# Performance work log

Measured on AMD Instinct MI355X. Metric: run time of the kernel, lower is better.

## Reference

```python
import jax, jax.numpy as jnp
import numpy as np

N, E, G = 50000, 400000, 256   # nodes, edges, graphs
DIN, DH = 513, 128             # int(256*4/2+1), dim_h
BN_EPS = 1e-5

def _lin_init(k, fin, fout):
    k1, k2 = jax.random.split(k)
    s = 1.0 / np.sqrt(fin)
    w = jax.random.uniform(k1, (fin, fout), jnp.float32, -s, s)
    b = jax.random.uniform(k2, (fout,), jnp.float32, -s, s)
    return w, b

def setup_inputs():
    ks = list(jax.random.split(jax.random.key(0), 20))
    inp = {
        'x': jax.random.normal(ks[0], (N, DIN), jnp.float32),
        'edge_index': jax.random.randint(ks[1], (2, E), 0, N),
        'batch': jnp.sort(jax.random.randint(ks[2], (N,), 0, G)),
    }
    i = 3
    for c in (1, 2, 3):
        fin = DIN if c == 1 else DH
        w1, b1 = _lin_init(ks[i], fin, DH); i += 1
        w2, b2 = _lin_init(ks[i], DH, DH); i += 1
        inp['conv%d_w1' % c], inp['conv%d_b1' % c] = w1, b1
        inp['conv%d_bn_g' % c] = jnp.ones((DH,), jnp.float32)
        inp['conv%d_bn_b' % c] = jnp.zeros((DH,), jnp.float32)
        inp['conv%d_bn_m' % c] = 0.1 * jax.random.normal(ks[i], (DH,), jnp.float32); i += 1
        inp['conv%d_bn_v' % c] = jax.random.uniform(ks[i], (DH,), jnp.float32, 0.5, 1.5); i += 1
        inp['conv%d_w2' % c], inp['conv%d_b2' % c] = w2, b2
    inp['lin1_w'], inp['lin1_b'] = _lin_init(ks[i], 3 * DH, 3 * DH); i += 1
    inp['lin2_w'], inp['lin2_b'] = _lin_init(ks[i], 3 * DH, 3)
    return inp

def _gin_conv(x, src, dst, w1, b1, g, bb, m, v, w2, b2):
    # GINConv, eps=0: MLP((1+eps)*x + sum_{j->i} x_j)
    agg = jax.ops.segment_sum(x[src], dst, num_segments=x.shape[0])
    h = (x + agg) @ w1 + b1
    h = (h - m) * jax.lax.rsqrt(v + BN_EPS) * g + bb   # BatchNorm1d (eval, running stats)
    h = jax.nn.relu(h)
    return jax.nn.relu(h @ w2 + b2)

def _mean_pool(h, batch, num_graphs):
    s = jax.ops.segment_sum(h, batch, num_segments=num_graphs)
    cnt = jax.ops.segment_sum(jnp.ones((h.shape[0],), h.dtype), batch, num_segments=num_graphs)
    return s / jnp.maximum(cnt, 1.0)[:, None]

def reference(x, edge_index, batch, conv1_w1, conv1_b1, conv1_bn_g, conv1_bn_b, conv1_bn_m, conv1_bn_v, conv1_w2, conv1_b2, conv2_w1, conv2_b1, conv2_bn_g, conv2_bn_b, conv2_bn_m, conv2_bn_v, conv2_w2, conv2_b2, conv3_w1, conv3_b1, conv3_bn_g, conv3_bn_b, conv3_bn_m, conv3_bn_v, conv3_w2, conv3_b2, lin1_w, lin1_b, lin2_w, lin2_b):
    src, dst = edge_index[0], edge_index[1]
    h1 = _gin_conv(x, src, dst, conv1_w1, conv1_b1, conv1_bn_g, conv1_bn_b, conv1_bn_m, conv1_bn_v, conv1_w2, conv1_b2)
    h2 = _gin_conv(h1, src, dst, conv2_w1, conv2_b1, conv2_bn_g, conv2_bn_b, conv2_bn_m, conv2_bn_v, conv2_w2, conv2_b2)
    h3 = _gin_conv(h2, src, dst, conv3_w1, conv3_b1, conv3_bn_g, conv3_bn_b, conv3_bn_m, conv3_bn_v, conv3_w2, conv3_b2)
    h = jnp.concatenate([_mean_pool(h1, batch, G), _mean_pool(h2, batch, G), _mean_pool(h3, batch, G)], axis=1)
    h = jax.nn.relu(h @ lin1_w + lin1_b)   # dropout p=0.5 is identity in eval mode
    return h @ lin2_w + lin2_b
```

## Files before the change

kernel.cpp:

```cpp
#include <hip/hip_runtime.h>

#define NN 50000
#define NE 400000
#define NG 256
#define BN_EPS 1e-5f
#define SCAN_E 8
#define SCAN_CHUNK 2048
#define SCAN_NB 25

#define WOFF_C1W1 0
#define WOFF_C2W1 73728
#define WOFF_C3W1 90112
#define WOFF_W2_1 106496
#define WOFF_W2_2 122880
#define WOFF_W2_3 139264
#define WTOTAL    155648

typedef __attribute__((ext_vector_type(4))) float f32x4;
typedef __bf16 bf16x8 __attribute__((ext_vector_type(8)));
typedef __bf16 bf16x4 __attribute__((ext_vector_type(4)));

__device__ __forceinline__ void mfma_bf16(f32x4& d, bf16x8 a, bf16x8 b) {
  asm volatile("v_mfma_f32_16x16x32_bf16 %0, %1, %2, %0" : "+v"(d) : "v"(a), "v"(b));
}

__global__ __launch_bounds__(256)
void wprep_all(const float* __restrict__ w10, const float* __restrict__ w11,
               const float* __restrict__ w12, const float* __restrict__ w20,
               const float* __restrict__ w21, const float* __restrict__ w22,
               __bf16* __restrict__ wh, __bf16* __restrict__ wl) {
  int idx = blockIdx.x * 256 + threadIdx.x;
  if (idx >= WTOTAL) return;
  const float* W; int K, Kpad, base;
  if (idx < WOFF_C2W1)      { W = w10; K = 513; Kpad = 576; base = WOFF_C1W1; }
  else if (idx < WOFF_C3W1) { W = w11; K = 128; Kpad = 128; base = WOFF_C2W1; }
  else if (idx < WOFF_W2_1) { W = w12; K = 128; Kpad = 128; base = WOFF_C3W1; }
  else if (idx < WOFF_W2_2) { W = w20; K = 128; Kpad = 128; base = WOFF_W2_1; }
  else if (idx < WOFF_W2_3) { W = w21; K = 128; Kpad = 128; base = WOFF_W2_2; }
  else                      { W = w22; K = 128; Kpad = 128; base = WOFF_W2_3; }
  int local = idx - base;
  int n = local & 127, k = local >> 7;
  float v = (k < K) ? W[(long)k * 128 + n] : 0.f;
  __bf16 h = (__bf16)v;
  wh[base + (long)n * Kpad + k] = h;
  wl[base + (long)n * Kpad + k] = (__bf16)(v - (float)h);
}

__global__ void bn_prep_all(
    const float* __restrict__ b10, const float* __restrict__ g0,
    const float* __restrict__ bb0, const float* __restrict__ m0, const float* __restrict__ v0,
    const float* __restrict__ b11, const float* __restrict__ g1,
    const float* __restrict__ bb1, const float* __restrict__ m1, const float* __restrict__ v1,
    const float* __restrict__ b12, const float* __restrict__ g2,
    const float* __restrict__ bb2, const float* __restrict__ m2, const float* __restrict__ v2,
    float* __restrict__ scale, float* __restrict__ shift) {
  int t = threadIdx.x;
  int layer = t >> 7, c = t & 127;
  const float* b1 = layer == 0 ? b10 : layer == 1 ? b11 : b12;
  const float* g  = layer == 0 ? g0  : layer == 1 ? g1  : g2;
  const float* bb = layer == 0 ? bb0 : layer == 1 ? bb1 : bb2;
  const float* m  = layer == 0 ? m0  : layer == 1 ? m1  : m2;
  const float* v  = layer == 0 ? v0  : layer == 1 ? v1  : v2;
  float s = g[c] * rsqrtf(v[c] + BN_EPS);
  scale[t] = s;
  shift[t] = (b1[c] - m[c]) * s + bb[c];
}

template<bool BIAS, bool RELU, bool OUT_SPLIT, bool A_FP32>
__global__ __launch_bounds__(256, 3)
void gemm_ws(const float* __restrict__ Af,
             const __bf16* __restrict__ Ah, const __bf16* __restrict__ Al,
             const __bf16* __restrict__ Wh, const __bf16* __restrict__ Wl,
             const float* __restrict__ bias, float* __restrict__ Cf,
             __bf16* __restrict__ Ch, __bf16* __restrict__ Cl,
             int M, int Kact, int Kpad) {
  __shared__ __align__(16) __bf16 bsh[128 * 64];
  __shared__ __align__(16) __bf16 bsl[128 * 64];
  const int t = threadIdx.x;
  const int wave = t >> 6, lane = t & 63;
  const int lr = lane & 15, kg = lane >> 4;
  const int r0 = blockIdx.x * 128 + wave * 32;

  bool okA[2];
  const float* apf[2];
  const __bf16 *aph[2], *apl[2];
#pragma unroll
  for (int mi = 0; mi < 2; ++mi) {
    int row = r0 + mi * 16 + lr;
    okA[mi] = row < M;
    long ro = okA[mi] ? (long)row : 0;
    if (A_FP32) { apf[mi] = Af + ro * Kact + kg * 8; aph[mi] = nullptr; apl[mi] = nullptr; }
    else { aph[mi] = Ah + ro * Kpad + kg * 8; apl[mi] = Al + ro * Kpad + kg * 8; apf[mi] = nullptr; }
  }

  f32x4 acc[2][8] = {};
  bf16x8 zero8;
#pragma unroll
  for (int j = 0; j < 8; ++j) zero8[j] = (__bf16)0.f;

  float f0[2][8], f1[2][8];
  bf16x8 a0h[2], a0l[2], a1h[2], a1l[2];

#define PF(F, AH, AL, KQ)                                                     \
  if (A_FP32) {                                                               \
    if ((KQ) + 32 <= Kact) {                                                  \
      _Pragma("unroll") for (int mi = 0; mi < 2; ++mi)                        \
      _Pragma("unroll") for (int j = 0; j < 8; ++j)                           \
        F[mi][j] = okA[mi] ? apf[mi][(KQ) + j] : 0.f;                         \
    } else {                                                                  \
      _Pragma("unroll") for (int mi = 0; mi < 2; ++mi)                        \
      _Pragma("unroll") for (int j = 0; j < 8; ++j) {                         \
        int k = (KQ) + kg * 8 + j;                                            \
        F[mi][j] = (okA[mi] && k < Kact) ? apf[mi][(KQ) + j] : 0.f;           \
      }                                                                       \
    }                                                                         \
  } else {                                                                    \
    _Pragma("unroll") for (int mi = 0; mi < 2; ++mi) {                        \
      AH[mi] = okA[mi] ? *(const bf16x8*)(aph[mi] + (KQ)) : zero8;            \
      AL[mi] = okA[mi] ? *(const bf16x8*)(apl[mi] + (KQ)) : zero8;            \
    }                                                                         \
  }

#define STEP(F, AH, AL, S)                                                    \
  {                                                                           \
    bf16x8 fah[2], fal[2];                                                    \
    if (A_FP32) {                                                             \
      _Pragma("unroll") for (int mi = 0; mi < 2; ++mi)                        \
      _Pragma("unroll") for (int j = 0; j < 8; ++j) {                         \
        __bf16 h = (__bf16)F[mi][j];                                          \
        fah[mi][j] = h; fal[mi][j] = (__bf16)(F[mi][j] - (float)h);           \
      }                                                                       \
    } else {                                                                  \
      _Pragma("unroll") for (int mi = 0; mi < 2; ++mi) {                      \
        fah[mi] = AH[mi]; fal[mi] = AL[mi];                                   \
      }                                                                       \
    }                                                                         \
    _Pragma("unroll") for (int ni = 0; ni < 8; ++ni) {                        \
      int col = ni * 16 + lr;                                                 \
      int po = ((S) * 4 + kg) ^ (lr & 7);                                     \
      bf16x8 fbh = *(const bf16x8*)&bsh[col * 64 + po * 8];                   \
      bf16x8 fbl = *(const bf16x8*)&bsl[col * 64 + po * 8];                   \
      _Pragma("unroll") for (int mi = 0; mi < 2; ++mi)                        \
        mfma_bf16(acc[mi][ni], fah[mi], fbh);                                 \
      _Pragma("unroll") for (int mi = 0; mi < 2; ++mi)                        \
        mfma_bf16(acc[mi][ni], fal[mi], fbh);                                 \
      _Pragma("unroll") for (int mi = 0; mi < 2; ++mi)                        \
        mfma_bf16(acc[mi][ni], fah[mi], fbl);                                 \
    }                                                                         \
  }

  PF(f0, a0h, a0l, 0);
  for (int kc0 = 0; kc0 < Kpad; kc0 += 64) {
    __syncthreads();
#pragma unroll
    for (int i = 0; i < 4; ++i) {
      int id = t + i * 256;
      int col = id >> 3, oct = id & 7;
      int po = oct ^ (col & 7);
      *(bf16x8*)&bsh[col * 64 + po * 8] =
          *(const bf16x8*)&Wh[(long)col * Kpad + kc0 + oct * 8];
      *(bf16x8*)&bsl[col * 64 + po * 8] =
          *(const bf16x8*)&Wl[(long)col * Kpad + kc0 + oct * 8];
    }
    __syncthreads();
    PF(f1, a1h, a1l, kc0 + 32);
    STEP(f0, a0h, a0l, 0);
    if (kc0 + 64 < Kpad) { PF(f0, a0h, a0l, kc0 + 64); }
    STEP(f1, a1h, a1l, 1);
  }
#undef PF
#undef STEP

#pragma unroll
  for (int mi = 0; mi < 2; ++mi) {
#pragma unroll
    for (int ni = 0; ni < 8; ++ni) {
      int col = ni * 16 + lr;
      float bv = BIAS ? bias[col] : 0.f;
#pragma unroll
      for (int r = 0; r < 4; ++r) {
        int row = r0 + mi * 16 + kg * 4 + r;
        if (row < M) {
          float v = acc[mi][ni][r] + bv;
          if (RELU) v = fmaxf(v, 0.f);
          if (OUT_SPLIT) {
            __bf16 h = (__bf16)v;
            Ch[(long)row * 128 + col] = h;
            Cl[(long)row * 128 + col] = (__bf16)(v - (float)h);
          } else {
            Cf[(long)row * 128 + col] = v;
          }
        }
      }
    }
  }
}

template<bool BIAS, bool RELU, bool OUT_SPLIT, bool A_FP32>
__global__ __launch_bounds__(512)
void gemm_bsp(const float* __restrict__ Af,
              const __bf16* __restrict__ Ah, const __bf16* __restrict__ Al,
              const __bf16* __restrict__ Wh, const __bf16* __restrict__ Wl,
              const float* __restrict__ bias, float* __restrict__ Cf,
              __bf16* __restrict__ Ch, __bf16* __restrict__ Cl,
              int M, int Kact, int Kpad) {
  __shared__ __align__(16) __bf16 ah[64 * 40];
  __shared__ __align__(16) __bf16 al[64 * 40];
  __shared__ __align__(16) __bf16 bh[128 * 40];
  __shared__ __align__(16) __bf16 bl[128 * 40];
  const int t = threadIdx.x;
  const int row0 = blockIdx.x * 64;
  const int wave = t >> 6, lane = t & 63;
  const int wr = wave >> 2, wc = wave & 3;
  const int lr = lane & 15, kg = lane >> 4;

  const int b_r = (t >> 2) & 127, b_ko = t & 3;
  const __bf16* bh_src = Wh + (long)b_r * Kpad + b_ko * 8;
  const __bf16* bl_src = Wl + (long)b_r * Kpad + b_ko * 8;
  __bf16* bh_dst = bh + b_r * 40 + b_ko * 8;
  __bf16* bl_dst = bl + b_r * 40 + b_ko * 8;

  f32x4 acc[2][2] = {};
  bf16x8 zero8;
#pragma unroll
  for (int j = 0; j < 8; ++j) zero8[j] = (__bf16)0.f;

  const int a_pl = t >> 8, a_r8 = (t >> 2) & 63, a_ko = t & 3;
  const __bf16* a_src = (a_pl ? Al : Ah) + (long)(row0 + a_r8) * Kpad + a_ko * 8;
  __bf16* a_dst = (a_pl ? al : ah) + a_r8 * 40 + a_ko * 8;
  const bool a_ok8 = (row0 + a_r8) < M;
  const int a_rf = t >> 3, a_kq = t & 7;
  const bool a_okf = (row0 + a_rf) < M;
  const float* af_src = Af + (long)(row0 + a_rf) * Kact + a_kq * 4;
  __bf16* ahf_dst = ah + a_rf * 40 + a_kq * 4;
  __bf16* alf_dst = al + a_rf * 40 + a_kq * 4;

  bf16x8 av;
  float fa[4];
  if (A_FP32) {
#pragma unroll
    for (int j = 0; j < 4; ++j) {
      int k = a_kq * 4 + j;
      fa[j] = (a_okf && k < Kact) ? af_src[j] : 0.f;
    }
  } else {
    av = a_ok8 ? *(const bf16x8*)a_src : zero8;
  }
  bf16x8 bv0 = *(const bf16x8*)bh_src;
  bf16x8 bv1 = *(const bf16x8*)bl_src;

  for (int k0 = 0; k0 < Kpad; k0 += 32) {
    __syncthreads();
    if (A_FP32) {
      bf16x4 hv, lv;
#pragma unroll
      for (int j = 0; j < 4; ++j) {
        __bf16 h = (__bf16)fa[j];
        hv[j] = h; lv[j] = (__bf16)(fa[j] - (float)h);
      }
      *(bf16x4*)ahf_dst = hv;
      *(bf16x4*)alf_dst = lv;
    } else {
      *(bf16x8*)a_dst = av;
    }
    *(bf16x8*)bh_dst = bv0;
    *(bf16x8*)bl_dst = bv1;
    __syncthreads();
    int k1 = k0 + 32;
    if (k1 < Kpad) {
      if (A_FP32) {
#pragma unroll
        for (int j = 0; j < 4; ++j) {
          int k = k1 + a_kq * 4 + j;
          fa[j] = (a_okf && k < Kact) ? af_src[k1 + j] : 0.f;
        }
      } else {
        av = a_ok8 ? *(const bf16x8*)(a_src + k1) : zero8;
      }
      bv0 = *(const bf16x8*)(bh_src + k1);
      bv1 = *(const bf16x8*)(bl_src + k1);
    }
    bf16x8 fah[2], fal[2], fbh[2], fbl[2];
#pragma unroll
    for (int mi = 0; mi < 2; ++mi) {
      int r = wr * 32 + mi * 16 + lr;
      fah[mi] = *(const bf16x8*)&ah[r * 40 + kg * 8];
      fal[mi] = *(const bf16x8*)&al[r * 40 + kg * 8];
    }
#pragma unroll
    for (int ni = 0; ni < 2; ++ni) {
      int c = wc * 32 + ni * 16 + lr;
      fbh[ni] = *(const bf16x8*)&bh[c * 40 + kg * 8];
      fbl[ni] = *(const bf16x8*)&bl[c * 40 + kg * 8];
    }
#pragma unroll
    for (int mi = 0; mi < 2; ++mi)
#pragma unroll
      for (int ni = 0; ni < 2; ++ni) {
        mfma_bf16(acc[mi][ni], fah[mi], fbh[ni]);
        mfma_bf16(acc[mi][ni], fal[mi], fbh[ni]);
        mfma_bf16(acc[mi][ni], fah[mi], fbl[ni]);
      }
  }
#pragma unroll
  for (int mi = 0; mi < 2; ++mi) {
#pragma unroll
    for (int ni = 0; ni < 2; ++ni) {
      int col = wc * 32 + ni * 16 + lr;
      float bv = BIAS ? bias[col] : 0.f;
#pragma unroll
      for (int r = 0; r < 4; ++r) {
        int row = row0 + wr * 32 + mi * 16 + kg * 4 + r;
        if (row < M) {
          float v = acc[mi][ni][r] + bv;
          if (RELU) v = fmaxf(v, 0.f);
          if (OUT_SPLIT) {
            __bf16 h = (__bf16)v;
            Ch[(long)row * 128 + col] = h;
            Cl[(long)row * 128 + col] = (__bf16)(v - (float)h);
          } else {
            Cf[(long)row * 128 + col] = v;
          }
        }
      }
    }
  }
}

__global__ __launch_bounds__(256)
void deg_count(const int* __restrict__ dst, int* __restrict__ deg, int E) {
  int e = blockIdx.x * 256 + threadIdx.x;
  if (e < E) atomicAdd(&deg[dst[e]], 1);
}

__global__ __launch_bounds__(256)
void scan_sums(const int* __restrict__ deg, int* __restrict__ bsum) {
  __shared__ int sm[256];
  int base = blockIdx.x * SCAN_CHUNK + threadIdx.x * SCAN_E;
  int s = 0;
#pragma unroll
  for (int k = 0; k < SCAN_E; ++k) { int i = base + k; if (i < NN) s += deg[i]; }
  sm[threadIdx.x] = s; __syncthreads();
  for (int off = 128; off > 0; off >>= 1) {
    if (threadIdx.x < off) sm[threadIdx.x] += sm[threadIdx.x + off];
    __syncthreads();
  }
  if (threadIdx.x == 0) bsum[blockIdx.x] = sm[0];
}

__global__ void scan_offs(const int* __restrict__ bsum, int* __restrict__ boff,
                          int* __restrict__ rowptr) {
  if (threadIdx.x == 0) {
    int run = 0;
    for (int i = 0; i < SCAN_NB; ++i) { boff[i] = run; run += bsum[i]; }
    rowptr[NN] = run;
  }
}

__global__ __launch_bounds__(256)
void scan_final(const int* __restrict__ boff, int* __restrict__ rowptr,
                int* __restrict__ cursor) {
  __shared__ int sm[256];
  int t = threadIdx.x;
  int base = blockIdx.x * SCAN_CHUNK + t * SCAN_E;
  int v[SCAN_E]; int s = 0;
#pragma unroll
  for (int k = 0; k < SCAN_E; ++k) { int i = base + k; v[k] = (i < NN) ? rowptr[i] : 0; s += v[k]; }
  sm[t] = s; __syncthreads();
  for (int off = 1; off < 256; off <<= 1) {
    int val = sm[t]; int add = (t >= off) ? sm[t - off] : 0;
    __syncthreads();
    sm[t] = val + add;
    __syncthreads();
  }
  int excl = (t == 0 ? 0 : sm[t - 1]) + boff[blockIdx.x];
#pragma unroll
  for (int k = 0; k < SCAN_E; ++k) {
    int i = base + k;
    if (i < NN) { rowptr[i] = excl; cursor[i] = excl; }
    excl += v[k];
  }
}

__global__ __launch_bounds__(256)
void scatter_csr(const int* __restrict__ src, const int* __restrict__ dst,
                 int* __restrict__ cursor, int* __restrict__ csr_src, int E) {
  int e = blockIdx.x * 256 + threadIdx.x;
  if (e < E) {
    int d = dst[e];
    int pos = atomicAdd(&cursor[d], 1);
    csr_src[pos] = src[e];
  }
}

__global__ __launch_bounds__(256)
void gather_bn_split(const __bf16* __restrict__ yh, const __bf16* __restrict__ yl,
                     const int* __restrict__ rowptr,
                     const int* __restrict__ csr_src, const float* __restrict__ scale,
                     const float* __restrict__ shift, __bf16* __restrict__ oh,
                     __bf16* __restrict__ ol) {
  const int grp = threadIdx.x >> 5;
  const int lane = threadIdx.x & 31;
  const int node = blockIdx.x * 8 + grp;
  if (node >= NN) return;
  int s = rowptr[node], e = rowptr[node + 1];
  bf16x4 sh4 = *(const bf16x4*)&yh[(long)node * 128 + lane * 4];
  bf16x4 sl4 = *(const bf16x4*)&yl[(long)node * 128 + lane * 4];
  float a0 = (float)sh4[0] + (float)sl4[0];
  float a1 = (float)sh4[1] + (float)sl4[1];
  float a2 = (float)sh4[2] + (float)sl4[2];
  float a3 = (float)sh4[3] + (float)sl4[3];
  float b0 = 0.f, b1 = 0.f, b2 = 0.f, b3 = 0.f;
  int i = s;
  for (; i + 3 < e; i += 4) {
    int s0 = csr_src[i], s1 = csr_src[i + 1], s2 = csr_src[i + 2], s3 = csr_src[i + 3];
    bf16x4 v0 = *(const bf16x4*)&yh[(long)s0 * 128 + lane * 4];
    bf16x4 v1 = *(const bf16x4*)&yh[(long)s1 * 128 + lane * 4];
    bf16x4 v2 = *(const bf16x4*)&yh[(long)s2 * 128 + lane * 4];
    bf16x4 v3 = *(const bf16x4*)&yh[(long)s3 * 128 + lane * 4];
    a0 += (float)v0[0]; a1 += (float)v0[1]; a2 += (float)v0[2]; a3 += (float)v0[3];
    b0 += (float)v1[0]; b1 += (float)v1[1]; b2 += (float)v1[2]; b3 += (float)v1[3];
    a0 += (float)v2[0]; a1 += (float)v2[1]; a2 += (float)v2[2]; a3 += (float)v2[3];
    b0 += (float)v3[0]; b1 += (float)v3[1]; b2 += (float)v3[2]; b3 += (float)v3[3];
  }
  for (; i < e; ++i) {
    int sn = csr_src[i];
    bf16x4 v = *(const bf16x4*)&yh[(long)sn * 128 + lane * 4];
    a0 += (float)v[0]; a1 += (float)v[1]; a2 += (float)v[2]; a3 += (float)v[3];
  }
  a0 += b0; a1 += b1; a2 += b2; a3 += b3;
  float4 sc = ((const float4*)scale)[lane];
  float4 sh = ((const float4*)shift)[lane];
  float o0 = fmaxf(a0 * sc.x + sh.x, 0.f);
  float o1 = fmaxf(a1 * sc.y + sh.y, 0.f);
  float o2 = fmaxf(a2 * sc.z + sh.z, 0.f);
  float o3 = fmaxf(a3 * sc.w + sh.w, 0.f);
  __bf16 h0 = (__bf16)o0, h1 = (__bf16)o1, h2 = (__bf16)o2, h3 = (__bf16)o3;
  bf16x4 hv, lv;
  hv[0] = h0; hv[1] = h1; hv[2] = h2; hv[3] = h3;
  lv[0] = (__bf16)(o0 - (float)h0); lv[1] = (__bf16)(o1 - (float)h1);
  lv[2] = (__bf16)(o2 - (float)h2); lv[3] = (__bf16)(o3 - (float)h3);
  *(bf16x4*)&oh[(long)node * 128 + lane * 4] = hv;
  *(bf16x4*)&ol[(long)node * 128 + lane * 4] = lv;
}

__global__ __launch_bounds__(128)
void pool_mean_split(const __bf16* __restrict__ h0h, const __bf16* __restrict__ h0l,
                     const __bf16* __restrict__ h1h, const __bf16* __restrict__ h1l,
                     const __bf16* __restrict__ h2h, const __bf16* __restrict__ h2l,
                     const int* __restrict__ batch, float* __restrict__ pooled) {
  __shared__ int se[2];
  int layer = blockIdx.y;
  const __bf16* hh = (layer == 0) ? h0h : (layer == 1) ? h1h : h2h;
  const __bf16* hl = (layer == 0) ? h0l : (layer == 1) ? h1l : h2l;
  int g = blockIdx.x, c = threadIdx.x;
  if (threadIdx.x < 2) {
    int target = g + (int)threadIdx.x;
    int lo = 0, hi = NN;
    while (lo < hi) {
      int mid = (lo + hi) >> 1;
      if (batch[mid] < target) lo = mid + 1; else hi = mid;
    }
    se[threadIdx.x] = lo;
  }
  __syncthreads();
  int s = se[0], e = se[1];
  float a0 = 0.f, a1 = 0.f, a2 = 0.f, a3 = 0.f;
  int i = s;
  for (; i + 3 < e; i += 4) {
    a0 += (float)hh[(long)i * 128 + c] + (float)hl[(long)i * 128 + c];
    a1 += (float)hh[(long)(i + 1) * 128 + c] + (float)hl[(long)(i + 1) * 128 + c];
    a2 += (float)hh[(long)(i + 2) * 128 + c] + (float)hl[(long)(i + 2) * 128 + c];
    a3 += (float)hh[(long)(i + 3) * 128 + c] + (float)hl[(long)(i + 3) * 128 + c];
  }
  for (; i < e; ++i)
    a0 += (float)hh[(long)i * 128 + c] + (float)hl[(long)i * 128 + c];
  float acc = (a0 + a1) + (a2 + a3);
  pooled[g * 384 + layer * 128 + c] = acc / fmaxf((float)(e - s), 1.f);
}

__global__ __launch_bounds__(384)
void lin1_k(const float* __restrict__ pooled, const float* __restrict__ w,
            const float* __restrict__ b, float* __restrict__ z) {
  __shared__ float pr[384];
  int mrow = blockIdx.x, t = threadIdx.x;
  pr[t] = pooled[mrow * 384 + t];
  __syncthreads();
  float acc = b[t];
  for (int k = 0; k < 384; ++k) acc += pr[k] * w[k * 384 + t];
  z[mrow * 384 + t] = fmaxf(acc, 0.f);
}

__global__ __launch_bounds__(192)
void lin2_k(const float* __restrict__ z, const float* __restrict__ w,
            const float* __restrict__ b, float* __restrict__ out) {
  int idx = blockIdx.x * 192 + threadIdx.x;
  if (idx >= NG * 3) return;
  int mrow = idx / 3, j = idx % 3;
  float acc = b[j];
  for (int k = 0; k < 384; ++k) acc += z[mrow * 384 + k] * w[k * 3 + j];
  out[idx] = acc;
}

extern "C" void kernel_launch(void* const* d_in, const int* in_sizes, int n_in,
                              void* d_out, int out_size, void* d_ws, size_t ws_size,
                              hipStream_t stream) {
  const float* x = (const float*)d_in[0];
  const int* ei = (const int*)d_in[1];
  const int* batch = (const int*)d_in[2];
  const int* srcv = ei;
  const int* dstv = ei + NE;
  const float* cw1[3] = {(const float*)d_in[3], (const float*)d_in[11], (const float*)d_in[19]};
  const float* cb1[3] = {(const float*)d_in[4], (const float*)d_in[12], (const float*)d_in[20]};
  const float* cg[3]  = {(const float*)d_in[5], (const float*)d_in[13], (const float*)d_in[21]};
  const float* cbb[3] = {(const float*)d_in[6], (const float*)d_in[14], (const float*)d_in[22]};
  const float* cm[3]  = {(const float*)d_in[7], (const float*)d_in[15], (const float*)d_in[23]};
  const float* cv[3]  = {(const float*)d_in[8], (const float*)d_in[16], (const float*)d_in[24]};
  const float* cw2[3] = {(const float*)d_in[9], (const float*)d_in[17], (const float*)d_in[25]};
  const float* cb2[3] = {(const float*)d_in[10], (const float*)d_in[18], (const float*)d_in[26]};
  const float* lin1_w = (const float*)d_in[27];
  const float* lin1_b = (const float*)d_in[28];
  const float* lin2_w = (const float*)d_in[29];
  const float* lin2_b = (const float*)d_in[30];

  const size_t NNF = (size_t)NN * 128;
  float* wsf = (float*)d_ws;
  __bf16* yh = (__bf16*)wsf;
  __bf16* yl = yh + NNF;
  __bf16* Xb = (__bf16*)(wsf + NNF);
  __bf16* gh = Xb;
  __bf16* gl = Xb + (size_t)6400000;
  __bf16* hh[3], *hl[3];
  for (int c = 0; c < 3; ++c) {
    hh[c] = Xb + (size_t)12800000 + (size_t)c * 12800000;
    hl[c] = hh[c] + (size_t)6400000;
  }
  float* misc = wsf + NNF + (size_t)25600000;
  float* pooled = misc;
  float* z      = pooled + (size_t)NG * 384;
  float* scale  = z + (size_t)NG * 384;
  float* shift  = scale + 384;
  __bf16* whbuf = (__bf16*)(shift + 384);
  __bf16* wlbuf = whbuf + (size_t)WTOTAL;
  int* rowptr   = (int*)(wlbuf + (size_t)WTOTAL);
  int* cursor   = rowptr + NN + 1;
  int* csr_src  = cursor + NN;
  int* bsum     = csr_src + NE;
  int* boff     = bsum + 32;

  hipMemsetAsync(rowptr, 0, (NN + 1) * sizeof(int), stream);
  deg_count<<<(NE + 255) / 256, 256, 0, stream>>>(dstv, rowptr, NE);
  scan_sums<<<SCAN_NB, 256, 0, stream>>>(rowptr, bsum);
  scan_offs<<<1, 64, 0, stream>>>(bsum, boff, rowptr);
  scan_final<<<SCAN_NB, 256, 0, stream>>>(boff, rowptr, cursor);
  scatter_csr<<<(NE + 255) / 256, 256, 0, stream>>>(srcv, dstv, cursor, csr_src, NE);

  wprep_all<<<(WTOTAL + 255) / 256, 256, 0, stream>>>(
      cw1[0], cw1[1], cw1[2], cw2[0], cw2[1], cw2[2], whbuf, wlbuf);
  bn_prep_all<<<1, 384, 0, stream>>>(
      cb1[0], cg[0], cbb[0], cm[0], cv[0],
      cb1[1], cg[1], cbb[1], cm[1], cv[1],
      cb1[2], cg[2], cbb[2], cm[2], cv[2], scale, shift);

  const int w1off[3] = {WOFF_C1W1, WOFF_C2W1, WOFF_C3W1};
  const int w2off[3] = {WOFF_W2_1, WOFF_W2_2, WOFF_W2_3};
  const int ws_grid  = (NN + 127) / 128;
  const int bsp_grid = (NN + 63) / 64;
  for (int c = 0; c < 3; ++c) {
    int K = (c == 0) ? 513 : 128;
    int Kpad = (c == 0) ? 576 : 128;
    const __bf16* w1h = whbuf + w1off[c];
    const __bf16* w1l = wlbuf + w1off[c];
    const __bf16* w2h = whbuf + w2off[c];
    const __bf16* w2l = wlbuf + w2off[c];
    if (c == 0)
      gemm_ws<false, false, true, true><<<ws_grid, 256, 0, stream>>>(
          x, nullptr, nullptr, w1h, w1l, nullptr, nullptr, yh, yl, NN, K, Kpad);
    else
      gemm_bsp<false, false, true, false><<<bsp_grid, 512, 0, stream>>>(
          nullptr, hh[c - 1], hl[c - 1], w1h, w1l, nullptr, nullptr, yh, yl, NN, 128, 128);
    gather_bn_split<<<(NN + 7) / 8, 256, 0, stream>>>(
        yh, yl, rowptr, csr_src, scale + (size_t)c * 128, shift + (size_t)c * 128, gh, gl);
    gemm_bsp<true, true, true, false><<<bsp_grid, 512, 0, stream>>>(
        nullptr, gh, gl, w2h, w2l, cb2[c], nullptr, hh[c], hl[c], NN, 128, 128);
  }
  pool_mean_split<<<dim3(NG, 3), 128, 0, stream>>>(hh[0], hl[0], hh[1], hl[1], hh[2], hl[2],
                                                   batch, pooled);
  lin1_k<<<NG, 384, 0, stream>>>(pooled, lin1_w, lin1_b, z);
  lin2_k<<<4, 192, 0, stream>>>(z, lin2_w, lin2_b, (float*)d_out);
}
```

Baseline: 347.9 us.

## Split first-layer GEMM along K into two blocks and combine partial sums

```diff
diff --git a/kernel.cpp b/kernel.cpp
--- a/kernel.cpp
+++ b/kernel.cpp
@@ -7,6 +7,7 @@
 #define SCAN_E 8
 #define SCAN_CHUNK 2048
 #define SCAN_NB 25
+#define KSPLIT 320
 
 #define WOFF_C1W1 0
 #define WOFF_C2W1 73728
@@ -80,6 +81,9 @@
   const int wave = t >> 6, lane = t & 63;
   const int lr = lane & 15, kg = lane >> 4;
   const int r0 = blockIdx.x * 128 + wave * 32;
+  const int kBeg = blockIdx.y ? KSPLIT : 0;
+  const int kEnd = blockIdx.y ? Kpad : (gridDim.y > 1 ? KSPLIT : Kpad);
+  float* Cfp = Cf + (long)blockIdx.y * (long)M * 128;
 
   bool okA[2];
   const float* apf[2];
@@ -149,8 +153,8 @@
     }                                                                         \
   }
 
-  PF(f0, a0h, a0l, 0);
-  for (int kc0 = 0; kc0 < Kpad; kc0 += 64) {
+  PF(f0, a0h, a0l, kBeg);
+  for (int kc0 = kBeg; kc0 < kEnd; kc0 += 64) {
     __syncthreads();
 #pragma unroll
     for (int i = 0; i < 4; ++i) {
@@ -165,7 +169,7 @@
     __syncthreads();
     PF(f1, a1h, a1l, kc0 + 32);
     STEP(f0, a0h, a0l, 0);
-    if (kc0 + 64 < Kpad) { PF(f0, a0h, a0l, kc0 + 64); }
+    if (kc0 + 64 < kEnd) { PF(f0, a0h, a0l, kc0 + 64); }
     STEP(f1, a1h, a1l, 1);
   }
 #undef PF
@@ -188,12 +192,29 @@
             Ch[(long)row * 128 + col] = h;
             Cl[(long)row * 128 + col] = (__bf16)(v - (float)h);
           } else {
-            Cf[(long)row * 128 + col] = v;
+            Cfp[(long)row * 128 + col] = v;
           }
         }
       }
     }
   }
+}
+
+__global__ __launch_bounds__(256)
+void combine_split(const float* __restrict__ y0, const float* __restrict__ y1,
+                   __bf16* __restrict__ yh, __bf16* __restrict__ yl, int n4) {
+  int i = blockIdx.x * 256 + threadIdx.x;
+  if (i >= n4) return;
+  float4 a = ((const float4*)y0)[i];
+  float4 b = ((const float4*)y1)[i];
+  float s0 = a.x + b.x, s1 = a.y + b.y, s2 = a.z + b.z, s3 = a.w + b.w;
+  __bf16 h0 = (__bf16)s0, h1 = (__bf16)s1, h2 = (__bf16)s2, h3 = (__bf16)s3;
+  bf16x4 hv, lv;
+  hv[0] = h0; hv[1] = h1; hv[2] = h2; hv[3] = h3;
+  lv[0] = (__bf16)(s0 - (float)h0); lv[1] = (__bf16)(s1 - (float)h1);
+  lv[2] = (__bf16)(s2 - (float)h2); lv[3] = (__bf16)(s3 - (float)h3);
+  *(bf16x4*)&yh[(long)i * 4] = hv;
+  *(bf16x4*)&yl[(long)i * 4] = lv;
 }
 
 template<bool BIAS, bool RELU, bool OUT_SPLIT, bool A_FP32>
@@ -535,6 +556,7 @@
     hh[c] = Xb + (size_t)12800000 + (size_t)c * 12800000;
     hl[c] = hh[c] + (size_t)6400000;
   }
+  float* y0 = (float*)hh[1];
   float* misc = wsf + NNF + (size_t)25600000;
   float* pooled = misc;
   float* z      = pooled + (size_t)NG * 384;
@@ -566,19 +588,20 @@
   const int w2off[3] = {WOFF_W2_1, WOFF_W2_2, WOFF_W2_3};
   const int ws_grid  = (NN + 127) / 128;
   const int bsp_grid = (NN + 63) / 64;
+  const int n4 = NN * 32;
   for (int c = 0; c < 3; ++c) {
-    int K = (c == 0) ? 513 : 128;
-    int Kpad = (c == 0) ? 576 : 128;
     const __bf16* w1h = whbuf + w1off[c];
     const __bf16* w1l = wlbuf + w1off[c];
     const __bf16* w2h = whbuf + w2off[c];
     const __bf16* w2l = wlbuf + w2off[c];
-    if (c == 0)
-      gemm_ws<false, false, true, true><<<ws_grid, 256, 0, stream>>>(
-          x, nullptr, nullptr, w1h, w1l, nullptr, nullptr, yh, yl, NN, K, Kpad);
-    else
+    if (c == 0) {
+      gemm_ws<false, false, false, true><<<dim3(ws_grid, 2), 256, 0, stream>>>(
+          x, nullptr, nullptr, w1h, w1l, nullptr, y0, nullptr, nullptr, NN, 513, 576);
+      combine_split<<<(n4 + 255) / 256, 256, 0, stream>>>(y0, y0 + NNF, yh, yl, n4);
+    } else {
       gemm_bsp<false, false, true, false><<<bsp_grid, 512, 0, stream>>>(
           nullptr, hh[c - 1], hl[c - 1], w1h, w1l, nullptr, nullptr, yh, yl, NN, 128, 128);
+    }
     gather_bn_split<<<(NN + 7) / 8, 256, 0, stream>>>(
         yh, yl, rowptr, csr_src, scale + (size_t)c * 128, shift + (size_t)c * 128, gh, gl);
     gemm_bsp<true, true, true, false><<<bsp_grid, 512, 0, stream>>>(
```

Measured after the change: 356.6 us. 1.03x slower.
